# Optimization experiments

Hardware: AMD Instinct MI355X
Metric: run time of the kernel (lower is better)

The kernel has to match this reference:

```python
import jax, jax.numpy as jnp
import numpy as np

BLOCK_SIZE = 128


def setup_inputs() -> dict:
    key = jax.random.key(0)
    kq, kk, kv = jax.random.split(key, 3)
    B, H, S, D = 2, 16, 4096, 64
    q = jax.random.normal(kq, (B, H, S, D), dtype=jnp.float32)
    k = jax.random.normal(kk, (B, H, S, D), dtype=jnp.float32)
    v = jax.random.normal(kv, (B, H, S, D), dtype=jnp.float32)
    return {"q": q, "k": k, "v": v}


def _flash_attn(q, k, v, block_size=BLOCK_SIZE):
    # Faithful translation of FlashAttentionImpl (use_fp8=False, causal=False,
    # mask=None, deterministic=True), including its exact online recurrence
    # (which uses exp(scores - block_max) rather than exp(scores - new_max)).
    B, H, Sq, D = q.shape
    Sk = k.shape[2]
    nb = Sk // block_size  # Sk divisible by block_size by construction
    scale = 1.0 / jnp.sqrt(jnp.asarray(D, q.dtype))

    # [nb, B, H, block, D] for scanning over K/V blocks
    kb = k.reshape(B, H, nb, block_size, D).transpose(2, 0, 1, 3, 4)
    vb = v.reshape(B, H, nb, block_size, D).transpose(2, 0, 1, 3, 4)

    o0 = jnp.zeros((B, H, Sq, D), dtype=q.dtype)
    n0 = jnp.zeros((B, H, Sq, 1), dtype=q.dtype)
    m0 = jnp.full((B, H, Sq, 1), -jnp.inf, dtype=q.dtype)

    def step(carry, blk):
        o_acc, norm_acc, m_acc = carry
        k_blk, v_blk = blk  # [B,H,block,D]
        scores = jnp.einsum('bhqd,bhkd->bhqk', q, k_blk,
                            precision=jax.lax.Precision.HIGHEST) * scale
        block_max = jnp.max(scores, axis=-1, keepdims=True)
        new_max = jnp.maximum(m_acc, block_max)
        exp_scale = jnp.exp(m_acc - new_max)
        exp_scores = jnp.exp(scores - block_max)
        norm_new = norm_acc * exp_scale + jnp.sum(exp_scores, axis=-1, keepdims=True)
        o_new = o_acc * exp_scale + jnp.einsum(
            'bhqk,bhkd->bhqd', exp_scores, v_blk,
            precision=jax.lax.Precision.HIGHEST)
        return (o_new, norm_new, new_max), None

    (o, norm, _), _ = jax.lax.scan(step, (o0, n0, m0), (kb, vb))
    return o / (norm + 1e-06)


def reference(q, k, v):
    return _flash_attn(q, k, v)
```

## Files before the change

kernel.cpp:

```cpp
#include <hip/hip_runtime.h>
#include <cstdint>
#include <cstddef>

typedef float     f32x16 __attribute__((ext_vector_type(16)));
typedef _Float16  f16x8  __attribute__((ext_vector_type(8)));
typedef __bf16    bf16x8 __attribute__((ext_vector_type(8)));
typedef unsigned  u32x2  __attribute__((ext_vector_type(2)));
typedef unsigned  u32x4  __attribute__((ext_vector_type(4)));

static_assert(sizeof(f16x8) == 16, "f16x8 must be 16B");

#define DEV __device__ __forceinline__

DEV unsigned short f2h_bits(float f) {
    _Float16 h = (_Float16)f;
    return __builtin_bit_cast(unsigned short, h);
}
DEV unsigned pack2h(float a, float b) {
    return (unsigned)f2h_bits(a) | ((unsigned)f2h_bits(b) << 16);
}
DEV unsigned cvt_pkrtz(float a, float b) {
    unsigned r;
    asm("v_cvt_pkrtz_f16_f32 %0, %1, %2" : "=v"(r) : "v"(a), "v"(b));
    return r;
}
DEV float exp2_hw(float x) {
    float r;
    asm("v_exp_f32 %0, %1" : "=v"(r) : "v"(x));
    return r;
}

DEV unsigned f2bf_bits(float f) {
    unsigned u = __builtin_bit_cast(unsigned, f);
    return ((u + 0x7fffu + ((u >> 16) & 1u)) >> 16) & 0xffffu;
}
DEV float bf2f(unsigned bits) {
    return __builtin_bit_cast(float, bits << 16);
}
DEV unsigned pack2(float a, float b) {
    return f2bf_bits(a) | (f2bf_bits(b) << 16);
}

typedef __attribute__((address_space(1))) const void gas_t;
typedef __attribute__((address_space(3))) void       las_t;
DEV void gload_lds16(const void* g, void* l) {
    __builtin_amdgcn_global_load_lds((gas_t*)g, (las_t*)l, 16, 0, 0);
}

constexpr int D     = 64;
constexpr int SLEN  = 4096;
constexpr int KBLK  = 128;
constexpr int NBLK  = SLEN / KBLK;
constexpr int QTILE = 128;
constexpr int VSTR  = 136;
constexpr int NBH   = 32;
constexpr size_t IMG = 8192;
constexpr size_t TEN = (size_t)NBH * NBLK * IMG;
constexpr float QSCALE = 0.125f * 1.4426950408889634f;

__global__ __launch_bounds__(256, 2)
void prep16(const float* __restrict__ Kg, const float* __restrict__ Vg,
            unsigned short* __restrict__ kf_g, unsigned short* __restrict__ vt_g)
{
    __shared__ __align__(16) unsigned short kstage[IMG];
    __shared__ __align__(16) unsigned short vstage[IMG];

    const int tid = threadIdx.x;
    const int kb  = blockIdx.x;
    const int bh  = blockIdx.y;
    const long base = (long)bh * SLEN * D;
    const int  kv0  = kb * KBLK;
    const size_t img = (size_t)(bh * NBLK + kb) * IMG;

#pragma unroll
    for (int i = 0; i < 8; ++i) {
        int idx = i * 256 + tid;
        int row = idx >> 4;
        int dq  = idx & 15;
        float4 x = *(const float4*)(Kg + base + (long)(kv0 + row) * D + dq * 4);
        u32x2 p;
        p.x = pack2h(x.x, x.y);
        p.y = pack2h(x.z, x.w);
        int chunk = (row >> 5) * 256 + (dq >> 2) * 64 + (((dq >> 1) & 1) * 32) + (row & 31);
        *(u32x2*)&kstage[chunk * 8 + (dq & 1) * 4] = p;
    }

    const int e  = tid & 3;
    const int e0 = e & 1, e1 = e >> 1;
    const int DQi = (tid >> 2) & 15;
    const int w   = tid >> 6;
#pragma unroll
    for (int i = 0; i < 8; ++i) {
        int KQ = (i * 4 + w) * 4;
        int DQ = DQi * 4;
        float4 x = *(const float4*)(Vg + base + (long)(kv0 + KQ + e) * D + DQ);
        float f0 = x.x, f1 = x.y, f2 = x.z, f3 = x.w;
        float sA0 = e0 ? f0 : f1, sA1 = e0 ? f2 : f3;
        float rA0 = __shfl_xor(sA0, 1, 64), rA1 = __shfl_xor(sA1, 1, 64);
        float A0 = e0 ? rA0 : f0, A1 = e0 ? f1 : rA0;
        float A2 = e0 ? rA1 : f2, A3 = e0 ? f3 : rA1;
        float sB0 = e1 ? A0 : A2, sB1 = e1 ? A1 : A3;
        float rB0 = __shfl_xor(sB0, 2, 64), rB1 = __shfl_xor(sB1, 2, 64);
        float B0 = e1 ? rB0 : A0, B1 = e1 ? rB1 : A1;
        float B2 = e1 ? A2 : rB0, B3 = e1 ? A3 : rB1;
        int d = DQ + e;
        u32x2 p;
        p.x = pack2h(B0, B1);
        p.y = pack2h(B2, B3);
        int off = d * 128 + (KQ ^ ((d & 7) << 3));
        *(u32x2*)&vstage[off] = p;
    }

    __syncthreads();

#pragma unroll
    for (int i = 0; i < 4; ++i) {
        size_t t8 = (size_t)(i * 256 + tid) * 8;
        *(u32x4*)&kf_g[img + t8] = *(const u32x4*)&kstage[t8];
        *(u32x4*)&vt_g[img + t8] = *(const u32x4*)&vstage[t8];
    }
}

__global__ __launch_bounds__(256, 2)
void fa_fwd4(const float* __restrict__ Qg,
             const unsigned short* __restrict__ kf_g,
             const unsigned short* __restrict__ vt_g,
             float* __restrict__ Og)
{
    __shared__ __align__(16) unsigned short kf_l0[IMG];
    __shared__ __align__(16) unsigned short vt_l0[IMG];
    __shared__ __align__(16) unsigned short kf_l1[IMG];
    __shared__ __align__(16) unsigned short vt_l1[IMG];

    const int tid = threadIdx.x;
    const int l   = tid & 63;
    const int w   = tid >> 6;
    const int h   = l >> 5;
    const int ln  = l & 31;

    const int  bh   = blockIdx.y;
    const long base = (long)bh * SLEN * D;
    const float* Qb = Qg + base;
    float*       Ob = Og + base;
    const unsigned short* kf_b = kf_g + (size_t)bh * NBLK * IMG;
    const unsigned short* vt_b = vt_g + (size_t)bh * NBLK * IMG;

    const int qrow = blockIdx.x * QTILE + w * 32 + ln;
    f16x8 qf[4];
#pragma unroll
    for (int c = 0; c < 4; ++c) {
        const float* qp = Qb + (long)qrow * D + c * 16 + h * 8;
        float4 x0 = *(const float4*)qp;
        float4 x1 = *(const float4*)(qp + 4);
        u32x4 H;
        H.x = pack2h(x0.x * QSCALE, x0.y * QSCALE);
        H.y = pack2h(x0.z * QSCALE, x0.w * QSCALE);
        H.z = pack2h(x1.x * QSCALE, x1.y * QSCALE);
        H.w = pack2h(x1.z * QSCALE, x1.w * QSCALE);
        qf[c] = __builtin_bit_cast(f16x8, H);
    }

    f32x16 oa0 = {};
    f32x16 oa1 = {};
    f32x16 st[4];

    float mrun = -INFINITY;
    float norm = 0.0f;

    const int so = (w * 64) * 8;
    const int go = so + l * 8;

    {
        const unsigned short* kfs = kf_b;
        const unsigned short* vts = vt_b;
#pragma unroll
        for (int i = 0; i < 4; ++i) {
            gload_lds16(kfs + go + i * 2048, &kf_l0[so + i * 2048]);
            gload_lds16(vts + go + i * 2048, &vt_l0[so + i * 2048]);
        }
    }
    __syncthreads();

#define FA_ITER(CURK, CURV, NXTK, NXTV, KB)                                     \
    do {                                                                        \
        if ((KB) + 1 < NBLK) {                                                  \
            const unsigned short* kfs = kf_b + (size_t)((KB) + 1) * IMG;        \
            const unsigned short* vts = vt_b + (size_t)((KB) + 1) * IMG;        \
            _Pragma("unroll")                                                   \
            for (int i = 0; i < 4; ++i) {                                       \
                gload_lds16(kfs + go + i * 2048, &NXTK[so + i * 2048]);         \
                gload_lds16(vts + go + i * 2048, &NXTV[so + i * 2048]);         \
            }                                                                   \
        }                                                                       \
        _Pragma("unroll")                                                       \
        for (int ki = 0; ki < 4; ++ki) {                                        \
            f32x16 acc = {};                                                    \
            _Pragma("unroll")                                                   \
            for (int c = 0; c < 4; ++c) {                                       \
                int ch = (ki * 4 + c) * 64 + l;                                 \
                f16x8 a = *(const f16x8*)&CURK[ch * 8];                         \
                acc = __builtin_amdgcn_mfma_f32_32x32x16_f16(a, qf[c], acc, 0, 0, 0); \
            }                                                                   \
            st[ki] = acc;                                                       \
        }                                                                       \
        float bm = -INFINITY;                                                   \
        _Pragma("unroll")                                                       \
        for (int ki = 0; ki < 4; ++ki)                                          \
            _Pragma("unroll")                                                   \
            for (int r = 0; r < 16; ++r) bm = fmaxf(bm, st[ki][r]);             \
        bm = fmaxf(bm, __shfl_xor(bm, 32, 64));                                 \
        float newm = fmaxf(mrun, bm);                                           \
        float sc   = exp2_hw(mrun - newm);                                      \
        mrun = newm;                                                            \
        float psum = 0.0f;                                                      \
        _Pragma("unroll")                                                       \
        for (int ki = 0; ki < 4; ++ki) {                                        \
            _Pragma("unroll")                                                   \
            for (int r = 0; r < 16; ++r) {                                      \
                float p = exp2_hw(st[ki][r] - bm);                              \
                st[ki][r] = p;                                                  \
                psum += p;                                                      \
            }                                                                   \
        }                                                                       \
        psum += __shfl_xor(psum, 32, 64);                                       \
        norm = norm * sc + psum;                                                \
        if (__any(sc != 1.0f)) {                                                \
            _Pragma("unroll")                                                   \
            for (int r = 0; r < 16; ++r) { oa0[r] *= sc; oa1[r] *= sc; }        \
        }                                                                       \
        f16x8 pf[8];                                                            \
        _Pragma("unroll")                                                       \
        for (int c = 0; c < 8; ++c) {                                           \
            int ki = c >> 1, half = c & 1;                                      \
            int rb = half * 8;                                                  \
            unsigned A0 = cvt_pkrtz(st[ki][rb + 0], st[ki][rb + 1]);            \
            unsigned A1 = cvt_pkrtz(st[ki][rb + 2], st[ki][rb + 3]);            \
            unsigned B0 = cvt_pkrtz(st[ki][rb + 4], st[ki][rb + 5]);            \
            unsigned B1 = cvt_pkrtz(st[ki][rb + 6], st[ki][rb + 7]);            \
            unsigned s0 = h ? A0 : B0;                                          \
            unsigned s1 = h ? A1 : B1;                                          \
            unsigned r0 = (unsigned)__shfl_xor((int)s0, 32, 64);                \
            unsigned r1 = (unsigned)__shfl_xor((int)s1, 32, 64);                \
            u32x4 f;                                                            \
            f.x = h ? r0 : A0;                                                  \
            f.y = h ? r1 : A1;                                                  \
            f.z = h ? B0 : r0;                                                  \
            f.w = h ? B1 : r1;                                                  \
            pf[c] = __builtin_bit_cast(f16x8, f);                               \
        }                                                                       \
        _Pragma("unroll")                                                       \
        for (int c = 0; c < 8; ++c) {                                           \
            const int kvo = c * 16 + h * 8;                                     \
            const int sa  = ln * 128 + (kvo ^ ((ln & 7) << 3));                 \
            f16x8 va = *(const f16x8*)&CURV[sa];                                \
            f16x8 vb = *(const f16x8*)&CURV[sa + 4096];                         \
            oa0 = __builtin_amdgcn_mfma_f32_32x32x16_f16(va, pf[c], oa0, 0, 0, 0); \
            oa1 = __builtin_amdgcn_mfma_f32_32x32x16_f16(vb, pf[c], oa1, 0, 0, 0); \
        }                                                                       \
        __syncthreads();                                                        \
    } while (0)

#pragma unroll 1
    for (int kb = 0; kb < NBLK; kb += 2) {
        FA_ITER(kf_l0, vt_l0, kf_l1, vt_l1, kb);
        FA_ITER(kf_l1, vt_l1, kf_l0, vt_l0, kb + 1);
    }
#undef FA_ITER

    float inv = 1.0f / (norm + 1e-6f);
    long  orow = (long)qrow * D;
#pragma unroll
    for (int rg = 0; rg < 4; ++rg) {
        int d0 = 8 * rg + 4 * h;
        float4 w0, w1;
        w0.x = oa0[4 * rg + 0] * inv;
        w0.y = oa0[4 * rg + 1] * inv;
        w0.z = oa0[4 * rg + 2] * inv;
        w0.w = oa0[4 * rg + 3] * inv;
        w1.x = oa1[4 * rg + 0] * inv;
        w1.y = oa1[4 * rg + 1] * inv;
        w1.z = oa1[4 * rg + 2] * inv;
        w1.w = oa1[4 * rg + 3] * inv;
        *(float4*)(Ob + orow + d0)      = w0;
        *(float4*)(Ob + orow + 32 + d0) = w1;
    }
}

__global__ __launch_bounds__(256, 2)
void fa_fwd(const float* __restrict__ Qg, const float* __restrict__ Kg,
            const float* __restrict__ Vg, float* __restrict__ Og)
{
    __shared__ __align__(16) unsigned short khi[KBLK * D];
    __shared__ __align__(16) unsigned short klo[KBLK * D];
    __shared__ __align__(16) unsigned short vt[D * VSTR];

    const int tid = threadIdx.x;
    const int l   = tid & 63;
    const int w   = tid >> 6;
    const int h   = l >> 5;
    const int ln  = l & 31;

    const int  bh   = blockIdx.y;
    const long base = (long)bh * SLEN * D;
    const float* Qb = Qg + base;
    const float* Kb = Kg + base;
    const float* Vb = Vg + base;
    float*       Ob = Og + base;

    const int qrow = blockIdx.x * QTILE + w * 32 + ln;
    bf16x8 qhi[4], qlo[4];
#pragma unroll
    for (int c = 0; c < 4; ++c) {
        const float* qp = Qb + (long)qrow * D + c * 16 + h * 8;
        float4 x0 = *(const float4*)qp;
        float4 x1 = *(const float4*)(qp + 4);
        float xs[8] = {x0.x, x0.y, x0.z, x0.w, x1.x, x1.y, x1.z, x1.w};
        unsigned hw[4], lw[4];
#pragma unroll
        for (int j = 0; j < 4; ++j) {
            float a = xs[2 * j] * 0.125f, b = xs[2 * j + 1] * 0.125f;
            unsigned ha = f2bf_bits(a), hb = f2bf_bits(b);
            lw[j] = f2bf_bits(a - bf2f(ha)) | (f2bf_bits(b - bf2f(hb)) << 16);
            hw[j] = ha | (hb << 16);
        }
        u32x4 H = {hw[0], hw[1], hw[2], hw[3]};
        u32x4 L = {lw[0], lw[1], lw[2], lw[3]};
        qhi[c] = __builtin_bit_cast(bf16x8, H);
        qlo[c] = __builtin_bit_cast(bf16x8, L);
    }

    f32x16 oa0 = {};
    f32x16 oa1 = {};
    f32x16 st[4];

    float mrun = -INFINITY;
    float norm = 0.0f;

    const int e  = tid & 3;
    const int e0 = e & 1, e1 = e >> 1;
    const int DQi = (tid >> 2) & 15;

#pragma unroll 1
    for (int kb = 0; kb < NBLK; ++kb) {
        const int kv0 = kb * KBLK;

#pragma unroll
        for (int i = 0; i < 4; ++i) {
            int chunk = i * 256 + tid;
            int ki  = chunk >> 8;
            int c   = (chunk >> 6) & 3;
            int cl  = chunk & 63;
            int row = ki * 32 + (cl & 31);
            int d0  = c * 16 + (cl >> 5) * 8;
            const float* kp = Kb + (long)(kv0 + row) * D + d0;
            float4 x0 = *(const float4*)kp;
            float4 x1 = *(const float4*)(kp + 4);
            float xs[8] = {x0.x, x0.y, x0.z, x0.w, x1.x, x1.y, x1.z, x1.w};
            unsigned hw[4], lw[4];
#pragma unroll
            for (int j = 0; j < 4; ++j) {
                float a = xs[2 * j], b = xs[2 * j + 1];
                unsigned ha = f2bf_bits(a), hb = f2bf_bits(b);
                lw[j] = f2bf_bits(a - bf2f(ha)) | (f2bf_bits(b - bf2f(hb)) << 16);
                hw[j] = ha | (hb << 16);
            }
            u32x4 H = {hw[0], hw[1], hw[2], hw[3]};
            u32x4 L = {lw[0], lw[1], lw[2], lw[3]};
            *(u32x4*)&khi[chunk * 8] = H;
            *(u32x4*)&klo[chunk * 8] = L;
        }

#pragma unroll
        for (int i = 0; i < 8; ++i) {
            int KQ = (i * 4 + w) * 4;
            int DQ = DQi * 4;
            float4 x = *(const float4*)(Vb + (long)(kv0 + KQ + e) * D + DQ);
            float f0 = x.x, f1 = x.y, f2 = x.z, f3 = x.w;
            float sA0 = e0 ? f0 : f1, sA1 = e0 ? f2 : f3;
            float rA0 = __shfl_xor(sA0, 1, 64), rA1 = __shfl_xor(sA1, 1, 64);
            float A0 = e0 ? rA0 : f0, A1 = e0 ? f1 : rA0;
            float A2 = e0 ? rA1 : f2, A3 = e0 ? f3 : rA1;
            float sB0 = e1 ? A0 : A2, sB1 = e1 ? A1 : A3;
            float rB0 = __shfl_xor(sB0, 2, 64), rB1 = __shfl_xor(sB1, 2, 64);
            float B0 = e1 ? rB0 : A0, B1 = e1 ? rB1 : A1;
            float B2 = e1 ? A2 : rB0, B3 = e1 ? A3 : rB1;
            u32x2 p;
            p.x = pack2(B0, B1);
            p.y = pack2(B2, B3);
            *(u32x2*)&vt[(DQ + e) * VSTR + KQ] = p;
        }

        __syncthreads();

#pragma unroll
        for (int ki = 0; ki < 4; ++ki) {
            f32x16 acc = {};
#pragma unroll
            for (int c = 0; c < 4; ++c) {
                int ch = (ki * 4 + c) * 64 + l;
                bf16x8 ah = *(const bf16x8*)&khi[ch * 8];
                bf16x8 al = *(const bf16x8*)&klo[ch * 8];
                acc = __builtin_amdgcn_mfma_f32_32x32x16_bf16(ah, qhi[c], acc, 0, 0, 0);
                acc = __builtin_amdgcn_mfma_f32_32x32x16_bf16(ah, qlo[c], acc, 0, 0, 0);
                acc = __builtin_amdgcn_mfma_f32_32x32x16_bf16(al, qhi[c], acc, 0, 0, 0);
            }
            st[ki] = acc;
        }

        float bm = -INFINITY;
#pragma unroll
        for (int ki = 0; ki < 4; ++ki)
#pragma unroll
            for (int r = 0; r < 16; ++r) bm = fmaxf(bm, st[ki][r]);
        bm = fmaxf(bm, __shfl_xor(bm, 32, 64));

        float newm = fmaxf(mrun, bm);
        float sc   = __expf(mrun - newm);
        mrun = newm;

        float psum = 0.0f;
#pragma unroll
        for (int ki = 0; ki < 4; ++ki) {
#pragma unroll
            for (int r = 0; r < 16; ++r) {
                float p = __expf(st[ki][r] - bm);
                st[ki][r] = p;
                psum += p;
            }
        }
        psum += __shfl_xor(psum, 32, 64);
        norm = norm * sc + psum;

#pragma unroll
        for (int r = 0; r < 16; ++r) { oa0[r] *= sc; oa1[r] *= sc; }

        bf16x8 pf[8];
#pragma unroll
        for (int c = 0; c < 8; ++c) {
            int ki = c >> 1, half = c & 1;
            int rb = half * 8;
            unsigned A0 = pack2(st[ki][rb + 0], st[ki][rb + 1]);
            unsigned A1 = pack2(st[ki][rb + 2], st[ki][rb + 3]);
            unsigned B0 = pack2(st[ki][rb + 4], st[ki][rb + 5]);
            unsigned B1 = pack2(st[ki][rb + 6], st[ki][rb + 7]);
            unsigned s0 = h ? A0 : B0;
            unsigned s1 = h ? A1 : B1;
            unsigned r0 = (unsigned)__shfl_xor((int)s0, 32, 64);
            unsigned r1 = (unsigned)__shfl_xor((int)s1, 32, 64);
            u32x4 f;
            f.x = h ? r0 : A0;
            f.y = h ? r1 : A1;
            f.z = h ? B0 : r0;
            f.w = h ? B1 : r1;
            pf[c] = __builtin_bit_cast(bf16x8, f);
        }

#pragma unroll
        for (int c = 0; c < 8; ++c) {
            const int kvo = c * 16 + h * 8;
            bf16x8 va = *(const bf16x8*)&vt[(ln)      * VSTR + kvo];
            bf16x8 vb = *(const bf16x8*)&vt[(32 + ln) * VSTR + kvo];
            oa0 = __builtin_amdgcn_mfma_f32_32x32x16_bf16(va, pf[c], oa0, 0, 0, 0);
            oa1 = __builtin_amdgcn_mfma_f32_32x32x16_bf16(vb, pf[c], oa1, 0, 0, 0);
        }

        __syncthreads();
    }

    float inv = 1.0f / (norm + 1e-6f);
    long  orow = (long)qrow * D;
#pragma unroll
    for (int rg = 0; rg < 4; ++rg) {
        int d0 = 8 * rg + 4 * h;
        float4 w0, w1;
        w0.x = oa0[4 * rg + 0] * inv;
        w0.y = oa0[4 * rg + 1] * inv;
        w0.z = oa0[4 * rg + 2] * inv;
        w0.w = oa0[4 * rg + 3] * inv;
        w1.x = oa1[4 * rg + 0] * inv;
        w1.y = oa1[4 * rg + 1] * inv;
        w1.z = oa1[4 * rg + 2] * inv;
        w1.w = oa1[4 * rg + 3] * inv;
        *(float4*)(Ob + orow + d0)      = w0;
        *(float4*)(Ob + orow + 32 + d0) = w1;
    }
}

extern "C" void kernel_launch(void* const* d_in, const int* in_sizes, int n_in,
                              void* d_out, int out_size, void* d_ws, size_t ws_size,
                              hipStream_t stream)
{
    (void)in_sizes; (void)n_in; (void)out_size;
    const float* q = (const float*)d_in[0];
    const float* k = (const float*)d_in[1];
    const float* v = (const float*)d_in[2];
    float*       o = (float*)d_out;

    const size_t need = 2 * TEN * sizeof(unsigned short);

    if (ws_size >= need) {
        unsigned short* kf_g = (unsigned short*)d_ws;
        unsigned short* vt_g = kf_g + TEN;

        dim3 pgrid(NBLK, NBH);
        hipLaunchKernelGGL(prep16, pgrid, dim3(256), 0, stream, k, v, kf_g, vt_g);

        dim3 grid(SLEN / QTILE, NBH);
        hipLaunchKernelGGL(fa_fwd4, grid, dim3(256), 0, stream, q, kf_g, vt_g, o);
    } else {
        dim3 grid(SLEN / QTILE, NBH);
        hipLaunchKernelGGL(fa_fwd, grid, dim3(256), 0, stream, q, k, v, o);
    }
}
```

Baseline: 308.4 us.

## Double Q tile to 512-thread blocks and split K/V prep into half-blocks

The attention kernel now uses 512-thread blocks covering 256 query rows. Each K/V tile loaded into LDS is therefore shared by twice as many query rows, halving the global-to-LDS traffic per query and the number of blocks. The prep kernel is split so each block converts half of a K/V tile, doubling its grid for more parallelism. The grid for the attention kernel shrinks to 512 blocks, which may leave the 256 CUs less evenly loaded, and the occupancy hint changes to 512x4.

```diff
diff --git a/kernel.cpp b/kernel.cpp
--- a/kernel.cpp
+++ b/kernel.cpp
@@ -51,31 +51,32 @@
 constexpr int SLEN  = 4096;
 constexpr int KBLK  = 128;
 constexpr int NBLK  = SLEN / KBLK;
-constexpr int QTILE = 128;
+constexpr int QTILE = 256;
 constexpr int VSTR  = 136;
 constexpr int NBH   = 32;
 constexpr size_t IMG = 8192;
 constexpr size_t TEN = (size_t)NBH * NBLK * IMG;
 constexpr float QSCALE = 0.125f * 1.4426950408889634f;
 
-__global__ __launch_bounds__(256, 2)
-void prep16(const float* __restrict__ Kg, const float* __restrict__ Vg,
-            unsigned short* __restrict__ kf_g, unsigned short* __restrict__ vt_g)
+__global__ __launch_bounds__(256)
+void prep16h(const float* __restrict__ Kg, const float* __restrict__ Vg,
+             unsigned short* __restrict__ kf_g, unsigned short* __restrict__ vt_g)
 {
     __shared__ __align__(16) unsigned short kstage[IMG];
     __shared__ __align__(16) unsigned short vstage[IMG];
 
-    const int tid = threadIdx.x;
-    const int kb  = blockIdx.x;
-    const int bh  = blockIdx.y;
+    const int tid  = threadIdx.x;
+    const int kb   = blockIdx.x >> 1;
+    const int half = blockIdx.x & 1;
+    const int bh   = blockIdx.y;
     const long base = (long)bh * SLEN * D;
     const int  kv0  = kb * KBLK;
     const size_t img = (size_t)(bh * NBLK + kb) * IMG;
 
 #pragma unroll
-    for (int i = 0; i < 8; ++i) {
+    for (int i = 0; i < 4; ++i) {
         int idx = i * 256 + tid;
-        int row = idx >> 4;
+        int row = half * 64 + (idx >> 4);
         int dq  = idx & 15;
         float4 x = *(const float4*)(Kg + base + (long)(kv0 + row) * D + dq * 4);
         u32x2 p;
@@ -87,12 +88,12 @@
 
     const int e  = tid & 3;
     const int e0 = e & 1, e1 = e >> 1;
-    const int DQi = (tid >> 2) & 15;
-    const int w   = tid >> 6;
-#pragma unroll
-    for (int i = 0; i < 8; ++i) {
-        int KQ = (i * 4 + w) * 4;
-        int DQ = DQi * 4;
+    const int DQi = (tid >> 2) & 7;
+    const int g8  = tid >> 5;
+#pragma unroll
+    for (int i = 0; i < 4; ++i) {
+        int KQ = (i * 8 + g8) * 4;
+        int DQ = half * 32 + DQi * 4;
         float4 x = *(const float4*)(Vg + base + (long)(kv0 + KQ + e) * D + DQ);
         float f0 = x.x, f1 = x.y, f2 = x.z, f3 = x.w;
         float sA0 = e0 ? f0 : f1, sA1 = e0 ? f2 : f3;
@@ -114,15 +115,16 @@
     __syncthreads();
 
 #pragma unroll
-    for (int i = 0; i < 4; ++i) {
-        size_t t8 = (size_t)(i * 256 + tid) * 8;
+    for (int i = 0; i < 2; ++i) {
+        size_t t8 = (size_t)(half * 512 + i * 256 + tid) * 8;
         *(u32x4*)&kf_g[img + t8] = *(const u32x4*)&kstage[t8];
-        *(u32x4*)&vt_g[img + t8] = *(const u32x4*)&vstage[t8];
-    }
-}
-
-__global__ __launch_bounds__(256, 2)
-void fa_fwd4(const float* __restrict__ Qg,
+        size_t v8 = (size_t)(half * 4096) + (size_t)(i * 256 + tid) * 8;
+        *(u32x4*)&vt_g[img + v8] = *(const u32x4*)&vstage[v8];
+    }
+}
+
+__global__ __launch_bounds__(512, 4)
+void fa_fwd5(const float* __restrict__ Qg,
              const unsigned short* __restrict__ kf_g,
              const unsigned short* __restrict__ vt_g,
              float* __restrict__ Og)
@@ -167,18 +169,15 @@
     float mrun = -INFINITY;
     float norm = 0.0f;
 
-    const int so = (w * 64) * 8;
-    const int go = so + l * 8;
-
-    {
-        const unsigned short* kfs = kf_b;
-        const unsigned short* vts = vt_b;
-#pragma unroll
-        for (int i = 0; i < 4; ++i) {
-            gload_lds16(kfs + go + i * 2048, &kf_l0[so + i * 2048]);
-            gload_lds16(vts + go + i * 2048, &vt_l0[so + i * 2048]);
-        }
-    }
+    const int so0 = (w * 64) * 8;
+    const int so1 = (512 + w * 64) * 8;
+    const int go0 = so0 + l * 8;
+    const int go1 = so1 + l * 8;
+
+    gload_lds16(kf_b + go0, &kf_l0[so0]);
+    gload_lds16(kf_b + go1, &kf_l0[so1]);
+    gload_lds16(vt_b + go0, &vt_l0[so0]);
+    gload_lds16(vt_b + go1, &vt_l0[so1]);
     __syncthreads();
 
 #define FA_ITER(CURK, CURV, NXTK, NXTV, KB)                                     \
@@ -186,11 +185,10 @@
         if ((KB) + 1 < NBLK) {                                                  \
             const unsigned short* kfs = kf_b + (size_t)((KB) + 1) * IMG;        \
             const unsigned short* vts = vt_b + (size_t)((KB) + 1) * IMG;        \
-            _Pragma("unroll")                                                   \
-            for (int i = 0; i < 4; ++i) {                                       \
-                gload_lds16(kfs + go + i * 2048, &NXTK[so + i * 2048]);         \
-                gload_lds16(vts + go + i * 2048, &NXTV[so + i * 2048]);         \
-            }                                                                   \
+            gload_lds16(kfs + go0, &NXTK[so0]);                                 \
+            gload_lds16(kfs + go1, &NXTK[so1]);                                 \
+            gload_lds16(vts + go0, &NXTV[so0]);                                 \
+            gload_lds16(vts + go1, &NXTV[so1]);                                 \
         }                                                                       \
         _Pragma("unroll")                                                       \
         for (int ki = 0; ki < 4; ++ki) {                                        \
@@ -307,7 +305,7 @@
     const float* Vb = Vg + base;
     float*       Ob = Og + base;
 
-    const int qrow = blockIdx.x * QTILE + w * 32 + ln;
+    const int qrow = blockIdx.x * 128 + w * 32 + ln;
     bf16x8 qhi[4], qlo[4];
 #pragma unroll
     for (int c = 0; c < 4; ++c) {
@@ -502,13 +500,13 @@
         unsigned short* kf_g = (unsigned short*)d_ws;
         unsigned short* vt_g = kf_g + TEN;
 
-        dim3 pgrid(NBLK, NBH);
-        hipLaunchKernelGGL(prep16, pgrid, dim3(256), 0, stream, k, v, kf_g, vt_g);
+        dim3 pgrid(2 * NBLK, NBH);
+        hipLaunchKernelGGL(prep16h, pgrid, dim3(256), 0, stream, k, v, kf_g, vt_g);
 
         dim3 grid(SLEN / QTILE, NBH);
-        hipLaunchKernelGGL(fa_fwd4, grid, dim3(256), 0, stream, q, kf_g, vt_g, o);
+        hipLaunchKernelGGL(fa_fwd5, grid, dim3(512), 0, stream, q, kf_g, vt_g, o);
     } else {
-        dim3 grid(SLEN / QTILE, NBH);
+        dim3 grid(SLEN / 128, NBH);
         hipLaunchKernelGGL(fa_fwd, grid, dim3(256), 0, stream, q, k, v, o);
     }
 }
```

New measurement: 384.3 us. 1.25x slower.
